# Optimization experiments

Hardware: AMD Instinct MI355X
Metric: run time of the kernel (lower is better)

Reference implementation:

```python
import jax, jax.numpy as jnp
import numpy as np
from jax import lax

EPS = 1e-5

def conv2d(x, w, b, pad):
    y = lax.conv_general_dilated(x, w, (1, 1), [(pad, pad), (pad, pad)],
                                 dimension_numbers=('NCHW', 'OIHW', 'NCHW'))
    return y + b[None, :, None, None]

def batchnorm(x, gamma, beta):
    mean = jnp.mean(x, axis=(0, 2, 3), keepdims=True)
    var = jnp.var(x, axis=(0, 2, 3), keepdims=True)  # biased, as torch BN training mode
    return gamma[None, :, None, None] * (x - mean) * lax.rsqrt(var + EPS) + beta[None, :, None, None]

def maxpool2(x):
    return lax.reduce_window(x, -jnp.inf, lax.max, (1, 1, 2, 2), (1, 1, 2, 2), 'VALID')

def upsample(x, s):
    N, C, H, W = x.shape
    return jax.image.resize(x, (N, C, H * s, W * s), method='bilinear')

def select_topvar(x, k=3):
    # per-sample, per-channel unbiased variance; gather top-k variance channels
    N, C, H, W = x.shape
    v = jnp.var(x.reshape(N, C, H * W), axis=-1, ddof=1)  # [N, C]
    _, idx = lax.top_k(v, k)                              # argsort(-v)[:k]
    return jnp.take_along_axis(x, idx[:, :, None, None], axis=1)

def setup_inputs() -> dict:
    key = jax.random.key(0)
    ks = jax.random.split(key, 16)
    n_channel, n_class = 10, 5
    d = {}
    d['x'] = jax.random.normal(ks[0], (16, n_channel, 512, 512), jnp.float32)
    sc = 0.1
    d['w_ext1'] = jax.random.normal(ks[1], (16, n_channel, 1, 1), jnp.float32) * sc
    d['b_ext1'] = jnp.zeros((16,), jnp.float32)
    d['g_ebn1'] = jnp.ones((16,), jnp.float32)
    d['be_ebn1'] = jnp.zeros((16,), jnp.float32)
    d['w_ext2'] = jax.random.normal(ks[2], (16, 16, 1, 1), jnp.float32) * sc
    d['b_ext2'] = jnp.zeros((16,), jnp.float32)
    d['g_ebn2'] = jnp.ones((16,), jnp.float32)
    d['be_ebn2'] = jnp.zeros((16,), jnp.float32)
    d['w_c1'] = jax.random.normal(ks[3], (8, 3, 3, 3), jnp.float32) * sc
    d['b_c1'] = jnp.zeros((8,), jnp.float32)
    d['w_c2'] = jax.random.normal(ks[4], (16, 8, 3, 3), jnp.float32) * sc
    d['b_c2'] = jnp.zeros((16,), jnp.float32)
    d['g_bn1'] = jnp.ones((16,), jnp.float32)
    d['be_bn1'] = jnp.zeros((16,), jnp.float32)
    d['g_bn2'] = jnp.ones((8,), jnp.float32)
    d['be_bn2'] = jnp.zeros((8,), jnp.float32)
    d['w_1k'] = jax.random.normal(ks[5], (n_class, 24, 1, 1), jnp.float32) * sc
    d['b_1k'] = jnp.zeros((n_class,), jnp.float32)
    return d

def reference(x, w_ext1, b_ext1, g_ebn1, be_ebn1, w_ext2, b_ext2, g_ebn2, be_ebn2,
              w_c1, b_c1, w_c2, b_c2, g_bn1, be_bn1, g_bn2, be_bn2, w_1k, b_1k):
    # bandExtract: 1x1 conv -> BN -> sigmoid, twice
    h = jax.nn.sigmoid(batchnorm(conv2d(x, w_ext1, b_ext1, 0), g_ebn1, be_ebn1))
    h = jax.nn.sigmoid(batchnorm(conv2d(h, w_ext2, b_ext2, 0), g_ebn2, be_ebn2))
    # featureSelect: keep 3 channels with largest per-sample variance
    x0 = select_topvar(h, 3)                                   # [N,3,H,W]
    x1 = maxpool2(jax.nn.sigmoid(conv2d(x0, w_c1, b_c1, 1)))   # [N,8,H/2,W/2]
    x2 = maxpool2(jax.nn.sigmoid(conv2d(x1, w_c2, b_c2, 1)))   # [N,16,H/4,W/4]
    x2 = batchnorm(jax.nn.relu(upsample(x2, 4)), g_bn1, be_bn1)  # [N,16,H,W]
    x1 = batchnorm(jax.nn.relu(upsample(x1, 2)), g_bn2, be_bn2)  # [N,8,H,W]
    merge = jnp.concatenate([x1, x2], axis=1)                    # [N,24,H,W]
    return conv2d(merge, w_1k, b_1k, 0)                          # [N,n_class,H,W]
```

## Files before the change

### kernel.cpp

```cpp
#include <hip/hip_runtime.h>
#include <math.h>

#define N_    16
#define CIN_  10
#define CB_   16
#define H_    512
#define W_    512
#define HW_   (512*512)
#define EPSF  1e-5f

__device__ __forceinline__ float sgm(float z){ return 1.0f/(1.0f+expf(-z)); }

__global__ void k_zero(double* __restrict__ p, int n){
  for (int i=threadIdx.x; i<n; i+=blockDim.x) p[i]=0.0;
}

__global__ void k_fin(const double* __restrict__ S, const float* __restrict__ g,
                      const float* __restrict__ be, float* __restrict__ AB,
                      int C, double invM){
  int c = threadIdx.x;
  if (c < C){
    double s=0.0,q=0.0;
    for (int n=0;n<N_;++n){ s+=S[(n*C+c)*2]; q+=S[(n*C+c)*2+1]; }
    double mean = s*invM;
    double var  = q*invM - mean*mean;
    float a = g[c]*rsqrtf((float)var + EPSF);
    AB[c]   = a;
    AB[C+c] = be[c] - (float)mean*a;
  }
}

__global__ __launch_bounds__(256) void k_stats1(
    const float* __restrict__ x, const float* __restrict__ w1, const float* __restrict__ b1,
    double* __restrict__ S1)
{
  const int n = blockIdx.y;
  const int base = blockIdx.x*4096;
  const float* xp = x + (size_t)n*CIN_*HW_;
  float sum[CB_], sq[CB_];
#pragma unroll
  for (int c=0;c<CB_;++c){ sum[c]=0.f; sq[c]=0.f; }
#pragma unroll 1
  for (int it=0; it<4; ++it){
    const int p = base + it*1024 + threadIdx.x*4;
    float4 xv[CIN_];
#pragma unroll
    for (int ci=0; ci<CIN_; ++ci)
      xv[ci] = *(const float4*)(xp + (size_t)ci*HW_ + p);
#pragma unroll
    for (int co=0; co<CB_; ++co){
      float bb = b1[co];
      float ox=bb, oy=bb, oz=bb, ow=bb;
#pragma unroll
      for (int ci=0; ci<CIN_; ++ci){
        float w = w1[co*CIN_+ci];
        ox += w*xv[ci].x; oy += w*xv[ci].y; oz += w*xv[ci].z; ow += w*xv[ci].w;
      }
      sum[co] += ox+oy+oz+ow;
      sq[co]  += ox*ox+oy*oy+oz*oz+ow*ow;
    }
  }
  __shared__ float red[4][CB_][2];
  const int lane = threadIdx.x & 63, wid = threadIdx.x >> 6;
#pragma unroll
  for (int c=0;c<CB_;++c){
    float s=sum[c], q=sq[c];
    for (int off=32; off>0; off>>=1){ s += __shfl_down(s,off); q += __shfl_down(q,off); }
    if (lane==0){ red[wid][c][0]=s; red[wid][c][1]=q; }
  }
  __syncthreads();
  if (threadIdx.x < CB_*2){
    int c = threadIdx.x>>1, k = threadIdx.x&1;
    float t = red[0][c][k]+red[1][c][k]+red[2][c][k]+red[3][c][k];
    atomicAdd(&S1[(n*CB_+c)*2+k], (double)t);
  }
}

__global__ __launch_bounds__(256) void k_band2(
    const float* __restrict__ x,
    const float* __restrict__ w1, const float* __restrict__ b1, const float* __restrict__ AB1,
    const float* __restrict__ w2, const float* __restrict__ b2,
    float* __restrict__ B, double* __restrict__ S2)
{
  const int n = blockIdx.y;
  const int base = blockIdx.x*4096;
  const float* xp = x + (size_t)n*CIN_*HW_;
  float* bp = B + (size_t)n*CB_*HW_;
  float sum[CB_], sq[CB_];
#pragma unroll
  for (int c=0;c<CB_;++c){ sum[c]=0.f; sq[c]=0.f; }
#pragma unroll 1
  for (int it=0; it<4; ++it){
    const int p = base + it*1024 + threadIdx.x*4;
    float4 xv[CIN_];
#pragma unroll
    for (int ci=0; ci<CIN_; ++ci)
      xv[ci] = *(const float4*)(xp + (size_t)ci*HW_ + p);
    float4 s[CB_];
#pragma unroll
    for (int co=0; co<CB_; ++co){
      float bb = b1[co];
      float ox=bb, oy=bb, oz=bb, ow=bb;
#pragma unroll
      for (int ci=0; ci<CIN_; ++ci){
        float w = w1[co*CIN_+ci];
        ox += w*xv[ci].x; oy += w*xv[ci].y; oz += w*xv[ci].z; ow += w*xv[ci].w;
      }
      const float a = AB1[co], sh = AB1[CB_+co];
      s[co].x = sgm(a*ox+sh); s[co].y = sgm(a*oy+sh);
      s[co].z = sgm(a*oz+sh); s[co].w = sgm(a*ow+sh);
    }
#pragma unroll
    for (int co=0; co<CB_; ++co){
      float bb = b2[co];
      float ox=bb, oy=bb, oz=bb, ow=bb;
#pragma unroll
      for (int ci=0; ci<CB_; ++ci){
        float w = w2[co*CB_+ci];
        ox += w*s[ci].x; oy += w*s[ci].y; oz += w*s[ci].z; ow += w*s[ci].w;
      }
      float4 o; o.x=ox; o.y=oy; o.z=oz; o.w=ow;
      *(float4*)(bp + (size_t)co*HW_ + p) = o;
      sum[co] += ox+oy+oz+ow;
      sq[co]  += ox*ox+oy*oy+oz*oz+ow*ow;
    }
  }
  __shared__ float red[4][CB_][2];
  const int lane = threadIdx.x & 63, wid = threadIdx.x >> 6;
#pragma unroll
  for (int c=0;c<CB_;++c){
    float s=sum[c], q=sq[c];
    for (int off=32; off>0; off>>=1){ s += __shfl_down(s,off); q += __shfl_down(q,off); }
    if (lane==0){ red[wid][c][0]=s; red[wid][c][1]=q; }
  }
  __syncthreads();
  if (threadIdx.x < CB_*2){
    int c = threadIdx.x>>1, k = threadIdx.x&1;
    float t = red[0][c][k]+red[1][c][k]+red[2][c][k]+red[3][c][k];
    atomicAdd(&S2[(n*CB_+c)*2+k], (double)t);
  }
}

__global__ __launch_bounds__(256) void k_bnsig(
    float* __restrict__ B, const float* __restrict__ AB2, double* __restrict__ SV)
{
  const int n = blockIdx.z, c = blockIdx.y;
  const float a = AB2[c], b = AB2[CB_+c];
  float* p = B + ((size_t)(n*CB_+c))*HW_ + blockIdx.x*4096;
  float sum=0.f, sq=0.f;
#pragma unroll 1
  for (int it=0; it<4; ++it){
    float4 v = *(float4*)(p + it*1024 + threadIdx.x*4);
    v.x = sgm(a*v.x+b); v.y = sgm(a*v.y+b); v.z = sgm(a*v.z+b); v.w = sgm(a*v.w+b);
    *(float4*)(p + it*1024 + threadIdx.x*4) = v;
    sum += v.x+v.y+v.z+v.w;
    sq  += v.x*v.x+v.y*v.y+v.z*v.z+v.w*v.w;
  }
  __shared__ float red[4][2];
  const int lane = threadIdx.x & 63, wid = threadIdx.x >> 6;
  for (int off=32; off>0; off>>=1){ sum += __shfl_down(sum,off); sq += __shfl_down(sq,off); }
  if (lane==0){ red[wid][0]=sum; red[wid][1]=sq; }
  __syncthreads();
  if (threadIdx.x < 2){
    int k = threadIdx.x;
    float t = red[0][k]+red[1][k]+red[2][k]+red[3][k];
    atomicAdd(&SV[(n*CB_+c)*2+k], (double)t);
  }
}

__global__ void k_topk(const double* __restrict__ SV, int* __restrict__ IDX){
  __shared__ double var[N_][CB_];
  int t = threadIdx.x;
  if (t < N_*CB_){
    int n=t>>4, c=t&15;
    double s=SV[t*2], q=SV[t*2+1];
    const double M = (double)HW_;
    var[n][c] = (q - s*s/M)/(M-1.0);
  }
  __syncthreads();
  if (t < N_){
    double v[CB_];
#pragma unroll
    for (int c=0;c<CB_;++c) v[c]=var[t][c];
    for (int k=0;k<3;++k){
      int bi=0; double bv=v[0];
#pragma unroll
      for (int c=1;c<CB_;++c) if (v[c]>bv){ bv=v[c]; bi=c; }
      IDX[t*3+k]=bi; v[bi]=-1e300;
    }
  }
}

__global__ __launch_bounds__(256) void k_conv1p(
    const float* __restrict__ B, const int* __restrict__ IDX,
    const float* __restrict__ w, const float* __restrict__ bias,
    float* __restrict__ X1)
{
  const int n = blockIdx.y, ho = blockIdx.x, wo = threadIdx.x;
  __shared__ int chs[3];
  if (threadIdx.x < 3) chs[threadIdx.x] = IDX[n*3+threadIdx.x];
  __syncthreads();
  float in[3][4][4];
#pragma unroll
  for (int k=0;k<3;++k){
    const float* pc = B + ((size_t)(n*CB_+chs[k]))*HW_;
#pragma unroll
    for (int dy=0;dy<4;++dy){
      int r = 2*ho-1+dy;
      bool rok = (r>=0 && r<H_);
#pragma unroll
      for (int dx=0;dx<4;++dx){
        int cc = 2*wo-1+dx;
        in[k][dy][dx] = (rok && cc>=0 && cc<W_) ? pc[(size_t)r*W_+cc] : 0.f;
      }
    }
  }
#pragma unroll
  for (int co=0;co<8;++co){
    float m = -1e30f;
#pragma unroll
    for (int py=0;py<2;++py)
#pragma unroll
    for (int px=0;px<2;++px){
      float acc = bias[co];
#pragma unroll
      for (int k=0;k<3;++k)
#pragma unroll
      for (int kh=0;kh<3;++kh)
#pragma unroll
      for (int kw=0;kw<3;++kw)
        acc += w[((co*3+k)*3+kh)*3+kw] * in[k][py+kh][px+kw];
      m = fmaxf(m, acc);
    }
    X1[((size_t)(n*8+co)*256 + ho)*256 + wo] = sgm(m);
  }
}

__global__ __launch_bounds__(256) void k_conv2p(
    const float* __restrict__ X1, const float* __restrict__ w, const float* __restrict__ bias,
    float* __restrict__ X2)
{
  const int n  = blockIdx.y;
  const int wo = threadIdx.x & 127;
  const int ho = blockIdx.x*2 + (threadIdx.x>>7);
  float acc[16][4];
#pragma unroll
  for (int co=0;co<16;++co){
    float bb = bias[co];
    acc[co][0]=bb; acc[co][1]=bb; acc[co][2]=bb; acc[co][3]=bb;
  }
#pragma unroll 1
  for (int ci=0; ci<8; ++ci){
    const float* p = X1 + ((size_t)(n*8+ci))*65536;
    float patch[4][4];
#pragma unroll
    for (int dy=0;dy<4;++dy){
      int r = 2*ho-1+dy;
      bool rok = (r>=0 && r<256);
#pragma unroll
      for (int dx=0;dx<4;++dx){
        int cc = 2*wo-1+dx;
        patch[dy][dx] = (rok && cc>=0 && cc<256) ? p[r*256+cc] : 0.f;
      }
    }
#pragma unroll
    for (int co=0;co<16;++co){
      const float* wp = w + (co*8+ci)*9;
#pragma unroll
      for (int py=0;py<2;++py)
#pragma unroll
      for (int px=0;px<2;++px){
        float a = acc[co][py*2+px];
#pragma unroll
        for (int kh=0;kh<3;++kh)
#pragma unroll
        for (int kw=0;kw<3;++kw)
          a += wp[kh*3+kw]*patch[py+kh][px+kw];
        acc[co][py*2+px] = a;
      }
    }
  }
#pragma unroll
  for (int co=0;co<16;++co){
    float m = fmaxf(fmaxf(acc[co][0],acc[co][1]), fmaxf(acc[co][2],acc[co][3]));
    X2[((size_t)(n*16+co)*128 + ho)*128 + wo] = sgm(m);
  }
}

__global__ __launch_bounds__(256) void k_stats_up4(
    const float* __restrict__ X2, double* __restrict__ SB1)
{
  const int n = blockIdx.z, c = blockIdx.y;
  const float* p = X2 + ((size_t)(n*16+c))*16384;
  const int id = blockIdx.x*256 + threadIdx.x;
  const int ho = id>>7, m = id&127;
  const int q = ho>>2, r = ho&3;
  int rA, rB; float wA;
  if (r==0){ rA=q-1; rB=q;   wA=0.375f; }
  else if (r==1){ rA=q-1; rB=q;   wA=0.125f; }
  else if (r==2){ rA=q;   rB=q+1; wA=0.875f; }
  else          { rA=q;   rB=q+1; wA=0.625f; }
  const float wB = 1.f-wA;
  rA = max(rA,0); rB = min(rB,127);
  const int c0 = max(m-1,0), c1 = m, c2 = min(m+1,127);
  const float* pa = p + rA*128; const float* pb = p + rB*128;
  float t0 = wA*pa[c0]+wB*pb[c0];
  float t1 = wA*pa[c1]+wB*pb[c1];
  float t2 = wA*pa[c2]+wB*pb[c2];
  float o0 = fmaxf(0.375f*t0+0.625f*t1, 0.f);
  float o1 = fmaxf(0.125f*t0+0.875f*t1, 0.f);
  float o2 = fmaxf(0.875f*t1+0.125f*t2, 0.f);
  float o3 = fmaxf(0.625f*t1+0.375f*t2, 0.f);
  float sum = o0+o1+o2+o3;
  float sq  = o0*o0+o1*o1+o2*o2+o3*o3;
  __shared__ float red[4][2];
  const int lane = threadIdx.x & 63, wid = threadIdx.x >> 6;
  for (int off=32; off>0; off>>=1){ sum += __shfl_down(sum,off); sq += __shfl_down(sq,off); }
  if (lane==0){ red[wid][0]=sum; red[wid][1]=sq; }
  __syncthreads();
  if (threadIdx.x < 2){
    int k = threadIdx.x;
    float t = red[0][k]+red[1][k]+red[2][k]+red[3][k];
    atomicAdd(&SB1[(n*16+c)*2+k], (double)t);
  }
}

__global__ __launch_bounds__(256) void k_stats_up2(
    const float* __restrict__ X1, double* __restrict__ SB2)
{
  const int n = blockIdx.z, c = blockIdx.y;
  const float* p = X1 + ((size_t)(n*8+c))*65536;
  const int id = blockIdx.x*256 + threadIdx.x;
  const int ho = id>>7, m = id&127;
  const int i = ho>>1, r = ho&1;
  int rA, rB; float wA;
  if (r==0){ rA=i-1; rB=i;   wA=0.25f; }
  else     { rA=i;   rB=i+1; wA=0.75f; }
  const float wB = 1.f-wA;
  rA = max(rA,0); rB = min(rB,255);
  const int c0 = max(2*m-1,0), c1 = 2*m, c2 = 2*m+1, c3 = min(2*m+2,255);
  const float* pa = p + rA*256; const float* pb = p + rB*256;
  float t0 = wA*pa[c0]+wB*pb[c0];
  float t1 = wA*pa[c1]+wB*pb[c1];
  float t2 = wA*pa[c2]+wB*pb[c2];
  float t3 = wA*pa[c3]+wB*pb[c3];
  float o0 = fmaxf(0.25f*t0+0.75f*t1, 0.f);
  float o1 = fmaxf(0.75f*t1+0.25f*t2, 0.f);
  float o2 = fmaxf(0.25f*t1+0.75f*t2, 0.f);
  float o3 = fmaxf(0.75f*t2+0.25f*t3, 0.f);
  float sum = o0+o1+o2+o3;
  float sq  = o0*o0+o1*o1+o2*o2+o3*o3;
  __shared__ float red[4][2];
  const int lane = threadIdx.x & 63, wid = threadIdx.x >> 6;
  for (int off=32; off>0; off>>=1){ sum += __shfl_down(sum,off); sq += __shfl_down(sq,off); }
  if (lane==0){ red[wid][0]=sum; red[wid][1]=sq; }
  __syncthreads();
  if (threadIdx.x < 2){
    int k = threadIdx.x;
    float t = red[0][k]+red[1][k]+red[2][k]+red[3][k];
    atomicAdd(&SB2[(n*8+c)*2+k], (double)t);
  }
}

__global__ __launch_bounds__(256) void k_final(
    const float* __restrict__ X1, const float* __restrict__ X2,
    const float* __restrict__ ABB1, const float* __restrict__ ABB2,
    const float* __restrict__ w1k, const float* __restrict__ b1k,
    float* __restrict__ out)
{
  const int n = blockIdx.y;
  const int id = blockIdx.x*256 + threadIdx.x;
  const int h = id>>7, m = id&127;
  float acc[5][4];
#pragma unroll
  for (int cls=0;cls<5;++cls){
    float bb = b1k[cls];
    acc[cls][0]=bb; acc[cls][1]=bb; acc[cls][2]=bb; acc[cls][3]=bb;
  }
  {
    const int i = h>>1, r = h&1;
    int rA,rB; float wA;
    if (r==0){ rA=i-1; rB=i;   wA=0.25f; } else { rA=i; rB=i+1; wA=0.75f; }
    const float wB = 1.f-wA;
    rA = max(rA,0); rB = min(rB,255);
    const int c0 = max(2*m-1,0), c1 = 2*m, c2 = 2*m+1, c3 = min(2*m+2,255);
#pragma unroll
    for (int c=0;c<8;++c){
      const float* p  = X1 + ((size_t)(n*8+c))*65536;
      const float* pa = p + rA*256; const float* pb = p + rB*256;
      float t0 = wA*pa[c0]+wB*pb[c0];
      float t1 = wA*pa[c1]+wB*pb[c1];
      float t2 = wA*pa[c2]+wB*pb[c2];
      float t3 = wA*pa[c3]+wB*pb[c3];
      float o0 = 0.25f*t0+0.75f*t1, o1 = 0.75f*t1+0.25f*t2;
      float o2 = 0.25f*t1+0.75f*t2, o3 = 0.75f*t2+0.25f*t3;
      const float a = ABB2[c], bb = ABB2[8+c];
      o0 = a*fmaxf(o0,0.f)+bb; o1 = a*fmaxf(o1,0.f)+bb;
      o2 = a*fmaxf(o2,0.f)+bb; o3 = a*fmaxf(o3,0.f)+bb;
#pragma unroll
      for (int cls=0;cls<5;++cls){
        float wv = w1k[cls*24+c];
        acc[cls][0]+=wv*o0; acc[cls][1]+=wv*o1; acc[cls][2]+=wv*o2; acc[cls][3]+=wv*o3;
      }
    }
  }
  {
    const int q = h>>2, r = h&3;
    int rA,rB; float wA;
    if (r==0){ rA=q-1; rB=q;   wA=0.375f; }
    else if (r==1){ rA=q-1; rB=q;   wA=0.125f; }
    else if (r==2){ rA=q;   rB=q+1; wA=0.875f; }
    else          { rA=q;   rB=q+1; wA=0.625f; }
    const float wB = 1.f-wA;
    rA = max(rA,0); rB = min(rB,127);
    const int c0 = max(m-1,0), c1 = m, c2 = min(m+1,127);
#pragma unroll
    for (int c=0;c<16;++c){
      const float* p  = X2 + ((size_t)(n*16+c))*16384;
      const float* pa = p + rA*128; const float* pb = p + rB*128;
      float t0 = wA*pa[c0]+wB*pb[c0];
      float t1 = wA*pa[c1]+wB*pb[c1];
      float t2 = wA*pa[c2]+wB*pb[c2];
      float o0 = 0.375f*t0+0.625f*t1;
      float o1 = 0.125f*t0+0.875f*t1;
      float o2 = 0.875f*t1+0.125f*t2;
      float o3 = 0.625f*t1+0.375f*t2;
      const float a = ABB1[c], bb = ABB1[16+c];
      o0 = a*fmaxf(o0,0.f)+bb; o1 = a*fmaxf(o1,0.f)+bb;
      o2 = a*fmaxf(o2,0.f)+bb; o3 = a*fmaxf(o3,0.f)+bb;
#pragma unroll
      for (int cls=0;cls<5;++cls){
        float wv = w1k[cls*24+8+c];
        acc[cls][0]+=wv*o0; acc[cls][1]+=wv*o1; acc[cls][2]+=wv*o2; acc[cls][3]+=wv*o3;
      }
    }
  }
#pragma unroll
  for (int cls=0;cls<5;++cls){
    float4 v; v.x=acc[cls][0]; v.y=acc[cls][1]; v.z=acc[cls][2]; v.w=acc[cls][3];
    *(float4*)(out + ((size_t)(n*5+cls))*HW_ + (size_t)h*W_ + 4*m) = v;
  }
}

extern "C" void kernel_launch(void* const* d_in, const int* in_sizes, int n_in,
                              void* d_out, int out_size, void* d_ws, size_t ws_size,
                              hipStream_t stream) {
  const float* x       = (const float*)d_in[0];
  const float* w_ext1  = (const float*)d_in[1];
  const float* b_ext1  = (const float*)d_in[2];
  const float* g_ebn1  = (const float*)d_in[3];
  const float* be_ebn1 = (const float*)d_in[4];
  const float* w_ext2  = (const float*)d_in[5];
  const float* b_ext2  = (const float*)d_in[6];
  const float* g_ebn2  = (const float*)d_in[7];
  const float* be_ebn2 = (const float*)d_in[8];
  const float* w_c1    = (const float*)d_in[9];
  const float* b_c1    = (const float*)d_in[10];
  const float* w_c2    = (const float*)d_in[11];
  const float* b_c2    = (const float*)d_in[12];
  const float* g_bn1   = (const float*)d_in[13];
  const float* be_bn1  = (const float*)d_in[14];
  const float* g_bn2   = (const float*)d_in[15];
  const float* be_bn2  = (const float*)d_in[16];
  const float* w_1k    = (const float*)d_in[17];
  const float* b_1k    = (const float*)d_in[18];
  float* outp = (float*)d_out;

  char* ws = (char*)d_ws;
  float* B  = (float*)ws;
  float* X1 = (float*)(ws + 268435456);
  float* X2 = (float*)(ws + 268435456 + 33554432);
  char*  sb = ws + 268435456 + 33554432 + 16777216;
  double* S1  = (double*)sb;
  double* S2  = S1  + 512;
  double* SV  = S2  + 512;
  double* SB1 = SV  + 512;
  double* SB2 = SB1 + 512;
  float*  AB1  = (float*)(SB2 + 256);
  float*  AB2  = AB1 + 32;
  float*  ABB1 = AB2 + 32;
  float*  ABB2 = ABB1 + 32;
  int*    IDX  = (int*)(ABB2 + 16);

  const double invM_bn = 1.0/4194304.0;

  k_zero<<<1,256,0,stream>>>(S1, 2304);
  k_stats1<<<dim3(64,16),256,0,stream>>>(x, w_ext1, b_ext1, S1);
  k_fin<<<1,64,0,stream>>>(S1, g_ebn1, be_ebn1, AB1, 16, invM_bn);
  k_band2<<<dim3(64,16),256,0,stream>>>(x, w_ext1, b_ext1, AB1, w_ext2, b_ext2, B, S2);
  k_fin<<<1,64,0,stream>>>(S2, g_ebn2, be_ebn2, AB2, 16, invM_bn);
  k_bnsig<<<dim3(64,16,16),256,0,stream>>>(B, AB2, SV);
  k_topk<<<1,256,0,stream>>>(SV, IDX);
  k_conv1p<<<dim3(256,16),256,0,stream>>>(B, IDX, w_c1, b_c1, X1);
  k_conv2p<<<dim3(64,16),256,0,stream>>>(X1, w_c2, b_c2, X2);
  k_stats_up4<<<dim3(256,16,16),256,0,stream>>>(X2, SB1);
  k_stats_up2<<<dim3(256,8,16),256,0,stream>>>(X1, SB2);
  k_fin<<<1,64,0,stream>>>(SB1, g_bn1, be_bn1, ABB1, 16, invM_bn);
  k_fin<<<1,64,0,stream>>>(SB2, g_bn2, be_bn2, ABB2, 8, invM_bn);
  k_final<<<dim3(256,16),256,0,stream>>>(X1, X2, ABB1, ABB2, w_1k, b_1k, outp);
}
```

Measured before the change: 906.4 us.

## Derive first BN stats from input covariance and defer second BN-sigmoid write

Replaces the first stats pass, which recomputed the 1x1 conv, with a pass that accumulates per-sample input sums and the 55 pairwise products. The BN1 mean and variance are then derived analytically in double precision from the conv weights. The BN2+sigmoid pass no longer writes B back; it only reads it for variance stats, and conv1p applies BN+sigmoid on the fly for the three selected channels. Sigmoid also switches to hardware exp2/rcp intrinsics. The aim is to cut about 256 MB of writes and some compute, at the cost of more register pressure in the covariance kernel and repeated sigmoid evaluation in conv1p.

```diff
diff --git a/kernel.cpp b/kernel.cpp
--- a/kernel.cpp
+++ b/kernel.cpp
@@ -9,10 +9,14 @@
 #define HW_   (512*512)
 #define EPSF  1e-5f
 
-__device__ __forceinline__ float sgm(float z){ return 1.0f/(1.0f+expf(-z)); }
+__device__ __forceinline__ float sgm(float z){
+  float e = __builtin_amdgcn_exp2f(z * -1.44269504088896f);
+  return __builtin_amdgcn_rcpf(1.0f + e);
+}
 
 __global__ void k_zero(double* __restrict__ p, int n){
-  for (int i=threadIdx.x; i<n; i+=blockDim.x) p[i]=0.0;
+  int i = blockIdx.x*256 + threadIdx.x;
+  if (i < n) p[i] = 0.0;
 }
 
 __global__ void k_fin(const double* __restrict__ S, const float* __restrict__ g,
@@ -30,13 +34,89 @@
   }
 }
 
-__global__ __launch_bounds__(256) void k_stats1(
-    const float* __restrict__ x, const float* __restrict__ w1, const float* __restrict__ b1,
-    double* __restrict__ S1)
+__global__ __launch_bounds__(256) void k_cov(
+    const float* __restrict__ x, double* __restrict__ SP)
 {
   const int n = blockIdx.y;
   const int base = blockIdx.x*4096;
   const float* xp = x + (size_t)n*CIN_*HW_;
+  float s[CIN_], p[55];
+#pragma unroll
+  for (int i=0;i<CIN_;++i) s[i]=0.f;
+#pragma unroll
+  for (int i=0;i<55;++i) p[i]=0.f;
+#pragma unroll 1
+  for (int it=0; it<4; ++it){
+    const int off = base + it*1024 + threadIdx.x*4;
+    float4 xv[CIN_];
+#pragma unroll
+    for (int ci=0; ci<CIN_; ++ci)
+      xv[ci] = *(const float4*)(xp + (size_t)ci*HW_ + off);
+#pragma unroll
+    for (int ci=0; ci<CIN_; ++ci)
+      s[ci] += xv[ci].x + xv[ci].y + xv[ci].z + xv[ci].w;
+    int k=0;
+#pragma unroll
+    for (int i=0;i<CIN_;++i)
+#pragma unroll
+      for (int j=i;j<CIN_;++j,++k)
+        p[k] += xv[i].x*xv[j].x + xv[i].y*xv[j].y + xv[i].z*xv[j].z + xv[i].w*xv[j].w;
+  }
+  __shared__ float red[4][65];
+  const int lane = threadIdx.x & 63, wid = threadIdx.x >> 6;
+#pragma unroll
+  for (int k=0;k<65;++k){
+    float v = (k<CIN_) ? s[k] : p[k-CIN_];
+    for (int o=32;o>0;o>>=1) v += __shfl_down(v,o);
+    if (lane==0) red[wid][k]=v;
+  }
+  __syncthreads();
+  if (threadIdx.x < 65){
+    float v = red[0][threadIdx.x]+red[1][threadIdx.x]+red[2][threadIdx.x]+red[3][threadIdx.x];
+    atomicAdd(&SP[n*65+threadIdx.x], (double)v);
+  }
+}
+
+__global__ void k_fin1(const double* __restrict__ SP, const float* __restrict__ w1,
+                       const float* __restrict__ b1, const float* __restrict__ g,
+                       const float* __restrict__ be, float* __restrict__ AB){
+  __shared__ double Sm[CIN_], Cv[55];
+  int t = threadIdx.x;
+  if (t < 65){
+    double s = 0.0;
+    for (int n=0;n<N_;++n) s += SP[n*65+t];
+    if (t < CIN_) Sm[t] = s; else Cv[t-CIN_] = s;
+  }
+  __syncthreads();
+  if (t < CB_){
+    const double M = 16.0*(double)HW_;
+    double b = (double)b1[t];
+    double wd[CIN_];
+    double lin = 0.0;
+    for (int i=0;i<CIN_;++i){ wd[i] = (double)w1[t*CIN_+i]; lin += wd[i]*Sm[i]/M; }
+    double mean = b + lin;
+    double ey2 = b*b + 2.0*b*lin;
+    int k=0;
+    for (int i=0;i<CIN_;++i)
+      for (int j=i;j<CIN_;++j,++k)
+        ey2 += (i==j ? 1.0 : 2.0) * wd[i]*wd[j]*(Cv[k]/M);
+    double var = ey2 - mean*mean;
+    float a = g[t]*rsqrtf((float)var + EPSF);
+    AB[t] = a;
+    AB[CB_+t] = be[t] - (float)mean*a;
+  }
+}
+
+__global__ __launch_bounds__(256) void k_band2(
+    const float* __restrict__ x,
+    const float* __restrict__ w1, const float* __restrict__ b1, const float* __restrict__ AB1,
+    const float* __restrict__ w2, const float* __restrict__ b2,
+    float* __restrict__ B, double* __restrict__ S2)
+{
+  const int n = blockIdx.y;
+  const int base = blockIdx.x*4096;
+  const float* xp = x + (size_t)n*CIN_*HW_;
+  float* bp = B + (size_t)n*CB_*HW_;
   float sum[CB_], sq[CB_];
 #pragma unroll
   for (int c=0;c<CB_;++c){ sum[c]=0.f; sq[c]=0.f; }
@@ -47,6 +127,7 @@
 #pragma unroll
     for (int ci=0; ci<CIN_; ++ci)
       xv[ci] = *(const float4*)(xp + (size_t)ci*HW_ + p);
+    float4 s[CB_];
 #pragma unroll
     for (int co=0; co<CB_; ++co){
       float bb = b1[co];
@@ -56,6 +137,21 @@
         float w = w1[co*CIN_+ci];
         ox += w*xv[ci].x; oy += w*xv[ci].y; oz += w*xv[ci].z; ow += w*xv[ci].w;
       }
+      const float a = AB1[co], sh = AB1[CB_+co];
+      s[co].x = sgm(a*ox+sh); s[co].y = sgm(a*oy+sh);
+      s[co].z = sgm(a*oz+sh); s[co].w = sgm(a*ow+sh);
+    }
+#pragma unroll
+    for (int co=0; co<CB_; ++co){
+      float bb = b2[co];
+      float ox=bb, oy=bb, oz=bb, ow=bb;
+#pragma unroll
+      for (int ci=0; ci<CB_; ++ci){
+        float w = w2[co*CB_+ci];
+        ox += w*s[ci].x; oy += w*s[ci].y; oz += w*s[ci].z; ow += w*s[ci].w;
+      }
+      float4 o; o.x=ox; o.y=oy; o.z=oz; o.w=ow;
+      *(float4*)(bp + (size_t)co*HW_ + p) = o;
       sum[co] += ox+oy+oz+ow;
       sq[co]  += ox*ox+oy*oy+oz*oz+ow*ow;
     }
@@ -72,87 +168,21 @@
   if (threadIdx.x < CB_*2){
     int c = threadIdx.x>>1, k = threadIdx.x&1;
     float t = red[0][c][k]+red[1][c][k]+red[2][c][k]+red[3][c][k];
-    atomicAdd(&S1[(n*CB_+c)*2+k], (double)t);
-  }
-}
-
-__global__ __launch_bounds__(256) void k_band2(
-    const float* __restrict__ x,
-    const float* __restrict__ w1, const float* __restrict__ b1, const float* __restrict__ AB1,
-    const float* __restrict__ w2, const float* __restrict__ b2,
-    float* __restrict__ B, double* __restrict__ S2)
-{
-  const int n = blockIdx.y;
-  const int base = blockIdx.x*4096;
-  const float* xp = x + (size_t)n*CIN_*HW_;
-  float* bp = B + (size_t)n*CB_*HW_;
-  float sum[CB_], sq[CB_];
-#pragma unroll
-  for (int c=0;c<CB_;++c){ sum[c]=0.f; sq[c]=0.f; }
-#pragma unroll 1
-  for (int it=0; it<4; ++it){
-    const int p = base + it*1024 + threadIdx.x*4;
-    float4 xv[CIN_];
-#pragma unroll
-    for (int ci=0; ci<CIN_; ++ci)
-      xv[ci] = *(const float4*)(xp + (size_t)ci*HW_ + p);
-    float4 s[CB_];
-#pragma unroll
-    for (int co=0; co<CB_; ++co){
-      float bb = b1[co];
-      float ox=bb, oy=bb, oz=bb, ow=bb;
-#pragma unroll
-      for (int ci=0; ci<CIN_; ++ci){
-        float w = w1[co*CIN_+ci];
-        ox += w*xv[ci].x; oy += w*xv[ci].y; oz += w*xv[ci].z; ow += w*xv[ci].w;
-      }
-      const float a = AB1[co], sh = AB1[CB_+co];
-      s[co].x = sgm(a*ox+sh); s[co].y = sgm(a*oy+sh);
-      s[co].z = sgm(a*oz+sh); s[co].w = sgm(a*ow+sh);
-    }
-#pragma unroll
-    for (int co=0; co<CB_; ++co){
-      float bb = b2[co];
-      float ox=bb, oy=bb, oz=bb, ow=bb;
-#pragma unroll
-      for (int ci=0; ci<CB_; ++ci){
-        float w = w2[co*CB_+ci];
-        ox += w*s[ci].x; oy += w*s[ci].y; oz += w*s[ci].z; ow += w*s[ci].w;
-      }
-      float4 o; o.x=ox; o.y=oy; o.z=oz; o.w=ow;
-      *(float4*)(bp + (size_t)co*HW_ + p) = o;
-      sum[co] += ox+oy+oz+ow;
-      sq[co]  += ox*ox+oy*oy+oz*oz+ow*ow;
-    }
-  }
-  __shared__ float red[4][CB_][2];
-  const int lane = threadIdx.x & 63, wid = threadIdx.x >> 6;
-#pragma unroll
-  for (int c=0;c<CB_;++c){
-    float s=sum[c], q=sq[c];
-    for (int off=32; off>0; off>>=1){ s += __shfl_down(s,off); q += __shfl_down(q,off); }
-    if (lane==0){ red[wid][c][0]=s; red[wid][c][1]=q; }
-  }
-  __syncthreads();
-  if (threadIdx.x < CB_*2){
-    int c = threadIdx.x>>1, k = threadIdx.x&1;
-    float t = red[0][c][k]+red[1][c][k]+red[2][c][k]+red[3][c][k];
     atomicAdd(&S2[(n*CB_+c)*2+k], (double)t);
   }
 }
 
-__global__ __launch_bounds__(256) void k_bnsig(
-    float* __restrict__ B, const float* __restrict__ AB2, double* __restrict__ SV)
+__global__ __launch_bounds__(256) void k_varstats(
+    const float* __restrict__ B, const float* __restrict__ AB2, double* __restrict__ SV)
 {
   const int n = blockIdx.z, c = blockIdx.y;
   const float a = AB2[c], b = AB2[CB_+c];
-  float* p = B + ((size_t)(n*CB_+c))*HW_ + blockIdx.x*4096;
+  const float* p = B + ((size_t)(n*CB_+c))*HW_ + blockIdx.x*4096;
   float sum=0.f, sq=0.f;
 #pragma unroll 1
   for (int it=0; it<4; ++it){
-    float4 v = *(float4*)(p + it*1024 + threadIdx.x*4);
+    float4 v = *(const float4*)(p + it*1024 + threadIdx.x*4);
     v.x = sgm(a*v.x+b); v.y = sgm(a*v.y+b); v.z = sgm(a*v.z+b); v.w = sgm(a*v.w+b);
-    *(float4*)(p + it*1024 + threadIdx.x*4) = v;
     sum += v.x+v.y+v.z+v.w;
     sq  += v.x*v.x+v.y*v.y+v.z*v.z+v.w*v.w;
   }
@@ -192,18 +222,25 @@
 }
 
 __global__ __launch_bounds__(256) void k_conv1p(
-    const float* __restrict__ B, const int* __restrict__ IDX,
+    const float* __restrict__ B, const int* __restrict__ IDX, const float* __restrict__ AB2,
     const float* __restrict__ w, const float* __restrict__ bias,
     float* __restrict__ X1)
 {
   const int n = blockIdx.y, ho = blockIdx.x, wo = threadIdx.x;
   __shared__ int chs[3];
-  if (threadIdx.x < 3) chs[threadIdx.x] = IDX[n*3+threadIdx.x];
+  __shared__ float ca[3], cb[3];
+  if (threadIdx.x < 3){
+    int c = IDX[n*3+threadIdx.x];
+    chs[threadIdx.x] = c;
+    ca[threadIdx.x] = AB2[c];
+    cb[threadIdx.x] = AB2[CB_+c];
+  }
   __syncthreads();
   float in[3][4][4];
 #pragma unroll
   for (int k=0;k<3;++k){
     const float* pc = B + ((size_t)(n*CB_+chs[k]))*HW_;
+    const float a = ca[k], bb = cb[k];
 #pragma unroll
     for (int dy=0;dy<4;++dy){
       int r = 2*ho-1+dy;
@@ -211,7 +248,7 @@
 #pragma unroll
       for (int dx=0;dx<4;++dx){
         int cc = 2*wo-1+dx;
-        in[k][dy][dx] = (rok && cc>=0 && cc<W_) ? pc[(size_t)r*W_+cc] : 0.f;
+        in[k][dy][dx] = (rok && cc>=0 && cc<W_) ? sgm(a*pc[(size_t)r*W_+cc]+bb) : 0.f;
       }
     }
   }
@@ -471,8 +508,8 @@
   float* X1 = (float*)(ws + 268435456);
   float* X2 = (float*)(ws + 268435456 + 33554432);
   char*  sb = ws + 268435456 + 33554432 + 16777216;
-  double* S1  = (double*)sb;
-  double* S2  = S1  + 512;
+  double* SP  = (double*)sb;
+  double* S2  = SP  + 1040;
   double* SV  = S2  + 512;
   double* SB1 = SV  + 512;
   double* SB2 = SB1 + 512;
@@ -484,14 +521,14 @@
 
   const double invM_bn = 1.0/4194304.0;
 
-  k_zero<<<1,256,0,stream>>>(S1, 2304);
-  k_stats1<<<dim3(64,16),256,0,stream>>>(x, w_ext1, b_ext1, S1);
-  k_fin<<<1,64,0,stream>>>(S1, g_ebn1, be_ebn1, AB1, 16, invM_bn);
+  k_zero<<<12,256,0,stream>>>(SP, 2832);
+  k_cov<<<dim3(64,16),256,0,stream>>>(x, SP);
+  k_fin1<<<1,128,0,stream>>>(SP, w_ext1, b_ext1, g_ebn1, be_ebn1, AB1);
   k_band2<<<dim3(64,16),256,0,stream>>>(x, w_ext1, b_ext1, AB1, w_ext2, b_ext2, B, S2);
   k_fin<<<1,64,0,stream>>>(S2, g_ebn2, be_ebn2, AB2, 16, invM_bn);
-  k_bnsig<<<dim3(64,16,16),256,0,stream>>>(B, AB2, SV);
+  k_varstats<<<dim3(64,16,16),256,0,stream>>>(B, AB2, SV);
   k_topk<<<1,256,0,stream>>>(SV, IDX);
-  k_conv1p<<<dim3(256,16),256,0,stream>>>(B, IDX, w_c1, b_c1, X1);
+  k_conv1p<<<dim3(256,16),256,0,stream>>>(B, IDX, AB2, w_c1, b_c1, X1);
   k_conv2p<<<dim3(64,16),256,0,stream>>>(X1, w_c2, b_c2, X2);
   k_stats_up4<<<dim3(256,16,16),256,0,stream>>>(X2, SB1);
   k_stats_up2<<<dim3(256,8,16),256,0,stream>>>(X1, SB2);
```

Measured after the change: 818.3 us. 9.7% less time.
